# Kernel optimization log

Hardware: AMD Instinct MI355X
Metric: run time of the kernel (lower is better)

Reference implementation:

```python
import jax, jax.numpy as jnp
import numpy as np
from jax import lax

EPS = 1e-5  # BatchNorm2d default eps


def binarize(v):
    # Hubara sign binarization with straight-through estimator:
    # forward = sign(v) (sign(0)=+1), backward grad = 1_{|v|<=1}
    vc = jnp.clip(v, -1.0, 1.0)
    s = jnp.where(v >= 0, 1.0, -1.0).astype(v.dtype)
    return vc + lax.stop_gradient(s - vc)


def setup_inputs() -> dict:
    key = jax.random.key(0)
    k1, k2 = jax.random.split(key)
    x = jax.random.normal(k1, (32, 256, 56, 56), dtype=jnp.float32)
    W = jax.random.normal(k2, (256, 256, 3, 3), dtype=jnp.float32) * 0.05
    gamma = jnp.ones((256,), dtype=jnp.float32)
    beta = jnp.zeros((256,), dtype=jnp.float32)
    return {"x": x, "W": W, "gamma": gamma, "beta": beta}


def reference(x, W, gamma, beta):
    # BnnActivation: binarize input to {-1,+1}
    bx = binarize(x)
    # BnnConv2d: binarize weights, dilated conv (stride=1, padding=2, dilation=2)
    bw = binarize(W)
    y = lax.conv_general_dilated(
        bx, bw,
        window_strides=(1, 1),
        padding=((2, 2), (2, 2)),
        rhs_dilation=(2, 2),
        dimension_numbers=("NCHW", "OIHW", "NCHW"),
    )  # [N, C_out, H, W]
    # BatchNorm2d (training-mode batch statistics, affine)
    mean = jnp.mean(y, axis=(0, 2, 3))
    var = jnp.var(y, axis=(0, 2, 3))
    yn = (y - mean[None, :, None, None]) * lax.rsqrt(var + EPS)[None, :, None, None]
    yn = yn * gamma[None, :, None, None] + beta[None, :, None, None]
    return jnp.tanh(yn)
```

## Files before the change

### kernel.cpp

```cpp
#include <hip/hip_runtime.h>

typedef unsigned long long u64;
typedef unsigned int u32;
typedef unsigned short u16;
typedef int i32x4 __attribute__((ext_vector_type(4)));
typedef int i32x16 __attribute__((ext_vector_type(16)));

#define HW 3136
#define XPITCH 3600
#define NPPIX 115200
#define KTOT 2304
#define MT 128
#define NSTEP 36


__global__ __launch_bounds__(256) void pack_w_i8(const float* __restrict__ W,
                                                 char* __restrict__ wp,
                                                 u64* __restrict__ ssum) {
    int idx = blockIdx.x * 256 + threadIdx.x;
    if (blockIdx.x == 0) {
        ssum[threadIdx.x] = 0;
        ssum[threadIdx.x + 256] = 0;
    }
    int ci4 = idx & 63;
    int tapco = idx >> 6;
    int co = tapco / 9, tap = tapco % 9;
    u32 out = 0;
    #pragma unroll
    for (int k = 0; k < 4; ++k) {
        float v = W[((size_t)co * 256 + ci4 * 4 + k) * 9 + tap];
        out |= (v >= 0.f ? 0x01u : 0xFFu) << (8 * k);
    }
    int kc = tap * 16 + (ci4 >> 2);
    *(u32*)(wp + ((long)kc * 256 + co) * 16 + (ci4 & 3) * 4) = out;
}

__global__ __launch_bounds__(256) void pack_x_i8(const float* __restrict__ x,
                                                 char* __restrict__ xp) {
    int s = blockIdx.x * 256 + threadIdx.x;
    int word = blockIdx.y;
    int n = s / XPITCH, p = s % XPITCH;
    int h = p / 60, w = p % 60;
    bool inb = (h >= 2 && h < 58 && w >= 2 && w < 58);
    u64 b = 0;
    if (inb) {
        const float* px = x + ((size_t)(n * 256 + word * 64)) * HW + (h - 2) * 56 + (w - 2);
        #pragma unroll 8
        for (int ci = 0; ci < 64; ++ci) {
            float v = px[(size_t)ci * HW];
            if (v >= 0.f) b |= 1ull << ci;
        }
    }
    #pragma unroll
    for (int q = 0; q < 4; ++q) {
        u32 wds[4];
        #pragma unroll
        for (int j = 0; j < 4; ++j) {
            u32 bits = (u32)(b >> (q * 16 + j * 4)) & 15u;
            u32 t = (bits * 0x00204081u) & 0x01010101u;
            wds[j] = inb ? (~(t * 0xFEu)) : 0u;
        }
        *(uint4*)(xp + (((long)(word * 4 + q)) * NPPIX + s) * 16) =
            make_uint4(wds[0], wds[1], wds[2], wds[3]);
    }
}

__global__ __launch_bounds__(512) void conv_mfma(const char* __restrict__ xp,
                                                 const char* __restrict__ wp,
                                                 short* __restrict__ y) {
    __shared__ char lds[2][24576];
    int tid = threadIdx.x;
    int lane = tid & 63, wid = tid >> 6;
    int wm = wid & 1, wn = wid >> 1;
    long tile = blockIdx.x;

    int xrow = tid & 127, xlc = tid >> 7;
    long s0 = tile * MT + xrow;
    int xn = (int)(s0 / HW), xhw = (int)(s0 % HW);
    long xpix = (long)xn * XPITCH + (xhw / 56) * 60 + (xhw % 56);

    i32x16 acc00 = {}, acc01 = {}, acc10 = {}, acc11 = {};

#define STAGE(step, buf)                                                                  \
    {                                                                                     \
        int tap = (step) >> 2, q = (step) & 3;                                            \
        long shift = (long)((tap / 3) * 120 + (tap % 3) * 2);                             \
        long xaddr = (((long)(q * 4 + xlc)) * NPPIX + xpix + shift) * 16;                 \
        __builtin_amdgcn_global_load_lds(                                                 \
            (const __attribute__((address_space(1))) u32*)(xp + xaddr),                   \
            (__attribute__((address_space(3))) u32*)&lds[buf][wid * 1024], 16, 0, 0);     \
        _Pragma("unroll")                                                                 \
        for (int r = 0; r < 2; ++r) {                                                     \
            int L = r * 512 + tid;                                                        \
            long waddr = (((long)(tap * 16 + q * 4 + (L >> 8))) * 256 + (L & 255)) * 16;  \
            __builtin_amdgcn_global_load_lds(                                             \
                (const __attribute__((address_space(1))) u32*)(wp + waddr),               \
                (__attribute__((address_space(3))) u32*)&lds[buf][8192 + (r * 512 + wid * 64) * 16], \
                16, 0, 0);                                                                \
        }                                                                                 \
    }

#define COMPUTE(buf)                                                                      \
    {                                                                                     \
        _Pragma("unroll")                                                                 \
        for (int kc = 0; kc < 2; ++kc) {                                                  \
            int cx = kc * 2 + (lane >> 5);                                                \
            const char* xb = &lds[buf][cx * 2048 + (wm * 64 + (lane & 31)) * 16];         \
            const char* wb = &lds[buf][8192 + cx * 4096 + (wn * 64 + (lane & 31)) * 16];  \
            i32x4 xf0 = *(const i32x4*)xb;                                                \
            i32x4 xf1 = *(const i32x4*)(xb + 512);                                        \
            i32x4 wf0 = *(const i32x4*)wb;                                                \
            i32x4 wf1 = *(const i32x4*)(wb + 512);                                        \
            acc00 = __builtin_amdgcn_mfma_i32_32x32x32_i8(wf0, xf0, acc00, 0, 0, 0);      \
            acc01 = __builtin_amdgcn_mfma_i32_32x32x32_i8(wf0, xf1, acc01, 0, 0, 0);      \
            acc10 = __builtin_amdgcn_mfma_i32_32x32x32_i8(wf1, xf0, acc10, 0, 0, 0);      \
            acc11 = __builtin_amdgcn_mfma_i32_32x32x32_i8(wf1, xf1, acc11, 0, 0, 0);      \
        }                                                                                 \
    }

    STAGE(0, 0);
    __syncthreads();
    #pragma unroll 2
    for (int st = 0; st < NSTEP; ++st) {
        int cur = st & 1;
        if (st + 1 < NSTEP) STAGE(st + 1, cur ^ 1);
        COMPUTE(cur);
        __syncthreads();
    }
#undef STAGE
#undef COMPUTE

    #pragma unroll
    for (int jp = 0; jp < 2; ++jp) {
        long s = tile * MT + wm * 64 + jp * 32 + (lane & 31);
        int n = (int)(s / HW), hw = (int)(s % HW);
        short* yb = y + ((long)n * 256) * HW + hw;
        #pragma unroll
        for (int jc = 0; jc < 2; ++jc) {
            i32x16 A = jc ? (jp ? acc11 : acc10) : (jp ? acc01 : acc00);
            #pragma unroll
            for (int r = 0; r < 16; ++r) {
                int co = wn * 64 + jc * 32 + (r & 3) + 8 * (r >> 2) + 4 * (lane >> 5);
                yb[(long)co * HW] = (short)A[r];
            }
        }
    }
}


__global__ __launch_bounds__(256) void stats1_kernel(const short* __restrict__ y,
                                                     u64* __restrict__ ssum) {
    int pl = blockIdx.x;
    const short* p = y + (size_t)pl * HW;
    int tid = threadIdx.x;
    int a1 = 0; long long q1 = 0;
    for (int i = tid; i < 392; i += 256) {
        int4 v = *(const int4*)(p + i * 8);
        int vs[4] = {v.x, v.y, v.z, v.w};
        int a = 0, q = 0;
        #pragma unroll
        for (int j = 0; j < 4; ++j) {
            int lo = (short)(vs[j] & 0xffff);
            int hi = (short)(vs[j] >> 16);
            a += lo + hi;
            q += lo * lo + hi * hi;
        }
        a1 += a; q1 += q;
    }
    long long s1 = a1, s2 = q1;
    #pragma unroll
    for (int off = 32; off > 0; off >>= 1) {
        s1 += __shfl_down(s1, off);
        s2 += __shfl_down(s2, off);
    }
    __shared__ long long ls1[4], ls2[4];
    if ((tid & 63) == 0) { ls1[tid >> 6] = s1; ls2[tid >> 6] = s2; }
    __syncthreads();
    if (tid == 0) {
        long long S1 = ls1[0] + ls1[1] + ls1[2] + ls1[3];
        long long S2 = ls2[0] + ls2[1] + ls2[2] + ls2[3];
        int cch = pl & 255;
        atomicAdd(&ssum[cch],       (u64)S1);
        atomicAdd(&ssum[256 + cch], (u64)S2);
    }
}

__global__ __launch_bounds__(256) void norm_kernel(const short* __restrict__ y,
                                                   const u64* __restrict__ ssum,
                                                   const float* __restrict__ gamma,
                                                   const float* __restrict__ beta,
                                                   float* __restrict__ out) {
    size_t i = ((size_t)blockIdx.x * 256 + threadIdx.x) * 8;
    int cch = (int)((i / HW) & 255);
    double S1 = (double)(long long)ssum[cch];
    double S2 = (double)(long long)ssum[256 + cch];
    double mean = S1 / 100352.0;
    double var = S2 / 100352.0 - mean * mean;
    float a = gamma[cch] * rsqrtf((float)var + 1e-5f);
    float b = beta[cch] - (float)mean * a;

    int4 v = *(const int4*)(y + i);
    int vs[4] = {v.x, v.y, v.z, v.w};
    float r[8];
    #pragma unroll
    for (int j = 0; j < 4; ++j) {
        short lo = (short)(vs[j] & 0xffff);
        short hi = (short)(vs[j] >> 16);
        r[2 * j]     = tanhf(a * (float)lo + b);
        r[2 * j + 1] = tanhf(a * (float)hi + b);
    }
    *(float4*)(out + i)     = make_float4(r[0], r[1], r[2], r[3]);
    *(float4*)(out + i + 4) = make_float4(r[4], r[5], r[6], r[7]);
}


__global__ __launch_bounds__(256) void pack_w_kernel(const float* __restrict__ W,
                                                     u32* __restrict__ wp32,
                                                     u16* __restrict__ pw,
                                                     u64* __restrict__ ssum) {
    if (blockIdx.x == 0) {
        ssum[threadIdx.x] = 0;
        ssum[threadIdx.x + 256] = 0;
    }
    int t = blockIdx.x * 256 + threadIdx.x;
    int co = t / 9, tap = t % 9;
    u64 b[4] = {0, 0, 0, 0};
    for (int ci = 0; ci < 256; ++ci) {
        float v = W[(size_t)(co * 256 + ci) * 9 + tap];
        if (v >= 0.f) b[ci >> 6] |= 1ull << (ci & 63);
    }
    u32* dst = wp32 + ((size_t)tap * 256 + co) * 8;
    #pragma unroll
    for (int j = 0; j < 4; ++j) {
        dst[2 * j]     = (u32)b[j];
        dst[2 * j + 1] = (u32)(b[j] >> 32);
    }
    pw[co * 9 + tap] = (u16)(__popcll(b[0]) + __popcll(b[1]) + __popcll(b[2]) + __popcll(b[3]));
}

__global__ __launch_bounds__(256) void pack_x_kernel(const float* __restrict__ x,
                                                     u64* __restrict__ xpad,
                                                     const u16* __restrict__ pw,
                                                     u16* __restrict__ bias) {
    int s = blockIdx.x * 256 + threadIdx.x;
    int word = blockIdx.y;
    int n = s / XPITCH, p = s % XPITCH;
    int h = p / 60, w = p % 60;
    u64 b = 0;
    if (h >= 2 && h < 58 && w >= 2 && w < 58) {
        const float* px = x + ((size_t)(n * 256 + word * 64)) * HW + (h - 2) * 56 + (w - 2);
        #pragma unroll 8
        for (int ci = 0; ci < 64; ++ci) {
            float v = px[(size_t)ci * HW];
            if (v >= 0.f) b |= 1ull << ci;
        }
    }
    xpad[(size_t)s * 4 + word] = b;

    if (blockIdx.x == 0 && blockIdx.y == 0) {
        for (int i = threadIdx.x; i < 9 * 256; i += 256) {
            int mi = i >> 8, co = i & 255;
            int rm = mi / 3, cm = mi % 3;
            int vr = rm == 0 ? 6 : (rm == 2 ? 3 : 7);
            int vc = cm == 0 ? 6 : (cm == 2 ? 3 : 7);
            int corr = 0;
            for (int kh = 0; kh < 3; ++kh)
                for (int kw = 0; kw < 3; ++kw)
                    if (!(((vr >> kh) & 1) && ((vc >> kw) & 1)))
                        corr += pw[co * 9 + kh * 3 + kw];
            bias[mi * 256 + co] = (u16)(256 * __popc(vr) * __popc(vc) + 2 * corr);
        }
    }
}

#define CPT 8
__global__ __launch_bounds__(256) void conv_kernel(const u32* __restrict__ xpad,
                                                   const u32* __restrict__ wp32,
                                                   const u16* __restrict__ bias,
                                                   short* __restrict__ y) {
    int s = blockIdx.x * 256 + threadIdx.x;
    int n = s / HW, hw = s % HW;
    int h = hw / 56, w = hw % 56;
    int co0 = blockIdx.y * CPT;
    const u32* xb = xpad + ((size_t)n * XPITCH + h * 60 + w) * 8;
    uint4 xa[9], xc[9];
    #pragma unroll
    for (int kh = 0; kh < 3; ++kh)
        #pragma unroll
        for (int kw = 0; kw < 3; ++kw) {
            const u32* px = xb + (kh * 120 + kw * 2) * 8;
            xa[kh * 3 + kw] = *(const uint4*)(px);
            xc[kh * 3 + kw] = *(const uint4*)(px + 4);
        }
    int acc[CPT];
    #pragma unroll
    for (int cc = 0; cc < CPT; ++cc) acc[cc] = 0;
    #pragma unroll
    for (int t = 0; t < 9; ++t) {
        const u32* wt = wp32 + (((size_t)t * 256 + co0) * 8);
        uint4 a = xa[t], b = xc[t];
        #pragma unroll
        for (int cc = 0; cc < CPT; ++cc) {
            const u32* wc8 = wt + cc * 8;
            acc[cc] = __popc(a.x ^ wc8[0]) + acc[cc];
            acc[cc] = __popc(a.y ^ wc8[1]) + acc[cc];
            acc[cc] = __popc(a.z ^ wc8[2]) + acc[cc];
            acc[cc] = __popc(a.w ^ wc8[3]) + acc[cc];
            acc[cc] = __popc(b.x ^ wc8[4]) + acc[cc];
            acc[cc] = __popc(b.y ^ wc8[5]) + acc[cc];
            acc[cc] = __popc(b.z ^ wc8[6]) + acc[cc];
            acc[cc] = __popc(b.w ^ wc8[7]) + acc[cc];
        }
    }
    int rm = (h < 2) ? 0 : (h > 53 ? 2 : 1);
    int cm = (w < 2) ? 0 : (w > 53 ? 2 : 1);
    int mi = rm * 3 + cm;
    uint4 bv = *(const uint4*)(bias + (size_t)mi * 256 + co0);
    u32 bw[4] = {bv.x, bv.y, bv.z, bv.w};
    short* yo = y + ((size_t)n * 256 + co0) * HW + hw;
    #pragma unroll
    for (int cc = 0; cc < CPT; ++cc) {
        int bval = (int)((bw[cc >> 1] >> ((cc & 1) * 16)) & 0xffff);
        yo[(size_t)cc * HW] = (short)(bval - 2 * acc[cc]);
    }
}


extern "C" void kernel_launch(void* const* d_in, const int* in_sizes, int n_in,
                              void* d_out, int out_size, void* d_ws, size_t ws_size,
                              hipStream_t stream) {
    const float* x     = (const float*)d_in[0];
    const float* W     = (const float*)d_in[1];
    const float* gamma = (const float*)d_in[2];
    const float* beta  = (const float*)d_in[3];
    float* out = (float*)d_out;
    char* ws = (char*)d_ws;

    short* y = (short*)ws;

    if (ws_size >= 81465344) {
        char* xi8 = ws + 51380224;
        char* wi8 = ws + 80871424;
        u64* ssum = (u64*)(ws + 81461248);
        pack_w_i8<<<576, 256, 0, stream>>>(W, wi8, ssum);
        pack_x_i8<<<dim3(450, 4), 256, 0, stream>>>(x, xi8);
        conv_mfma<<<784, 512, 0, stream>>>(xi8, wi8, y);
        stats1_kernel<<<8192, 256, 0, stream>>>(y, ssum);
        norm_kernel<<<12544, 256, 0, stream>>>(y, ssum, gamma, beta, out);
    } else {
        u64* xpad = (u64*)(ws + 51380224);
        u32* wp32 = (u32*)(ws + 55066624);
        u16* pw   = (u16*)(ws + 55140352);
        u16* bias = (u16*)(ws + 55144960);
        u64* ssum = (u64*)(ws + 55149568);
        pack_w_kernel<<<9, 256, 0, stream>>>(W, wp32, pw, ssum);
        pack_x_kernel<<<dim3(450, 4), 256, 0, stream>>>(x, xpad, pw, bias);
        conv_kernel<<<dim3(392, 32), 256, 0, stream>>>((const u32*)xpad, wp32, bias, y);
        stats1_kernel<<<8192, 256, 0, stream>>>(y, ssum);
        norm_kernel<<<12544, 256, 0, stream>>>(y, ssum, gamma, beta, out);
    }
}
```

Measured before the change: 140.8 us.

## Fuse BN statistics into conv epilogue and deepen load pipeline with manual waitcnt

The conv kernel now computes per-channel sum and sum-of-squares from its int accumulators with lane shuffles and atomics, so the separate stats kernel no longer re-reads y. The main loop is also restructured to keep two stages in flight, using explicit vmcnt/lgkmcnt waits and raw s_barrier in place of __syncthreads. The pipelining relies on the STAGE macro issuing exactly the load count that vmcnt(3) assumes, which is fragile, and the epilogue adds many global atomics.

Result: slower. 283.7 us (+101.5%).

```diff
diff --git a/kernel.cpp b/kernel.cpp
--- a/kernel.cpp
+++ b/kernel.cpp
@@ -67,7 +67,8 @@
 
 __global__ __launch_bounds__(512) void conv_mfma(const char* __restrict__ xp,
                                                  const char* __restrict__ wp,
-                                                 short* __restrict__ y) {
+                                                 short* __restrict__ y,
+                                                 u64* __restrict__ ssum) {
     __shared__ char lds[2][24576];
     int tid = threadIdx.x;
     int lane = tid & 63, wid = tid >> 6;
@@ -119,16 +120,23 @@
     }
 
     STAGE(0, 0);
-    __syncthreads();
+    STAGE(1, 1);
     #pragma unroll 2
-    for (int st = 0; st < NSTEP; ++st) {
+    for (int st = 0; st < NSTEP - 1; ++st) {
         int cur = st & 1;
-        if (st + 1 < NSTEP) STAGE(st + 1, cur ^ 1);
+        asm volatile("s_waitcnt vmcnt(3)" ::: "memory");
+        __builtin_amdgcn_s_barrier();
+        __builtin_amdgcn_sched_barrier(0);
         COMPUTE(cur);
-        __syncthreads();
-    }
-#undef STAGE
-#undef COMPUTE
+        __builtin_amdgcn_sched_barrier(0);
+        asm volatile("s_waitcnt lgkmcnt(0)" ::: "memory");
+        __builtin_amdgcn_s_barrier();
+        if (st + 2 < NSTEP) STAGE(st + 2, cur);
+    }
+    asm volatile("s_waitcnt vmcnt(0)" ::: "memory");
+    __builtin_amdgcn_s_barrier();
+    __builtin_amdgcn_sched_barrier(0);
+    COMPUTE((NSTEP - 1) & 1);
 
     #pragma unroll
     for (int jp = 0; jp < 2; ++jp) {
@@ -145,45 +153,29 @@
             }
         }
     }
-}
-
-
-__global__ __launch_bounds__(256) void stats1_kernel(const short* __restrict__ y,
-                                                     u64* __restrict__ ssum) {
-    int pl = blockIdx.x;
-    const short* p = y + (size_t)pl * HW;
-    int tid = threadIdx.x;
-    int a1 = 0; long long q1 = 0;
-    for (int i = tid; i < 392; i += 256) {
-        int4 v = *(const int4*)(p + i * 8);
-        int vs[4] = {v.x, v.y, v.z, v.w};
-        int a = 0, q = 0;
-        #pragma unroll
-        for (int j = 0; j < 4; ++j) {
-            int lo = (short)(vs[j] & 0xffff);
-            int hi = (short)(vs[j] >> 16);
-            a += lo + hi;
-            q += lo * lo + hi * hi;
-        }
-        a1 += a; q1 += q;
-    }
-    long long s1 = a1, s2 = q1;
-    #pragma unroll
-    for (int off = 32; off > 0; off >>= 1) {
-        s1 += __shfl_down(s1, off);
-        s2 += __shfl_down(s2, off);
-    }
-    __shared__ long long ls1[4], ls2[4];
-    if ((tid & 63) == 0) { ls1[tid >> 6] = s1; ls2[tid >> 6] = s2; }
-    __syncthreads();
-    if (tid == 0) {
-        long long S1 = ls1[0] + ls1[1] + ls1[2] + ls1[3];
-        long long S2 = ls2[0] + ls2[1] + ls2[2] + ls2[3];
-        int cch = pl & 255;
-        atomicAdd(&ssum[cch],       (u64)S1);
-        atomicAdd(&ssum[256 + cch], (u64)S2);
-    }
-}
+
+    #pragma unroll
+    for (int jc = 0; jc < 2; ++jc) {
+        i32x16 A0 = jc ? acc10 : acc00;
+        i32x16 A1 = jc ? acc11 : acc01;
+        #pragma unroll
+        for (int r = 0; r < 16; ++r) {
+            int v = A0[r] + A1[r];
+            int q = A0[r] * A0[r] + A1[r] * A1[r];
+            #pragma unroll
+            for (int off = 16; off > 0; off >>= 1) {
+                v += __shfl_xor(v, off);
+                q += __shfl_xor(q, off);
+            }
+            if ((lane & 31) == 0) {
+                int co = wn * 64 + jc * 32 + (r & 3) + 8 * (r >> 2) + 4 * (lane >> 5);
+                atomicAdd(&ssum[co],       (u64)(long long)v);
+                atomicAdd(&ssum[256 + co], (u64)(long long)q);
+            }
+        }
+    }
+}
+
 
 __global__ __launch_bounds__(256) void norm_kernel(const short* __restrict__ y,
                                                    const u64* __restrict__ ssum,
@@ -211,6 +203,43 @@
     }
     *(float4*)(out + i)     = make_float4(r[0], r[1], r[2], r[3]);
     *(float4*)(out + i + 4) = make_float4(r[4], r[5], r[6], r[7]);
+}
+
+__global__ __launch_bounds__(256) void stats1_kernel(const short* __restrict__ y,
+                                                     u64* __restrict__ ssum) {
+    int pl = blockIdx.x;
+    const short* p = y + (size_t)pl * HW;
+    int tid = threadIdx.x;
+    int a1 = 0; long long q1 = 0;
+    for (int i = tid; i < 392; i += 256) {
+        int4 v = *(const int4*)(p + i * 8);
+        int vs[4] = {v.x, v.y, v.z, v.w};
+        int a = 0, q = 0;
+        #pragma unroll
+        for (int j = 0; j < 4; ++j) {
+            int lo = (short)(vs[j] & 0xffff);
+            int hi = (short)(vs[j] >> 16);
+            a += lo + hi;
+            q += lo * lo + hi * hi;
+        }
+        a1 += a; q1 += q;
+    }
+    long long s1 = a1, s2 = q1;
+    #pragma unroll
+    for (int off = 32; off > 0; off >>= 1) {
+        s1 += __shfl_down(s1, off);
+        s2 += __shfl_down(s2, off);
+    }
+    __shared__ long long ls1[4], ls2[4];
+    if ((tid & 63) == 0) { ls1[tid >> 6] = s1; ls2[tid >> 6] = s2; }
+    __syncthreads();
+    if (tid == 0) {
+        long long S1 = ls1[0] + ls1[1] + ls1[2] + ls1[3];
+        long long S2 = ls2[0] + ls2[1] + ls2[2] + ls2[3];
+        int cch = pl & 255;
+        atomicAdd(&ssum[cch],       (u64)S1);
+        atomicAdd(&ssum[256 + cch], (u64)S2);
+    }
 }
 
 
@@ -344,8 +373,7 @@
         u64* ssum = (u64*)(ws + 81461248);
         pack_w_i8<<<576, 256, 0, stream>>>(W, wi8, ssum);
         pack_x_i8<<<dim3(450, 4), 256, 0, stream>>>(x, xi8);
-        conv_mfma<<<784, 512, 0, stream>>>(xi8, wi8, y);
-        stats1_kernel<<<8192, 256, 0, stream>>>(y, ssum);
+        conv_mfma<<<784, 512, 0, stream>>>(xi8, wi8, y, ssum);
         norm_kernel<<<12544, 256, 0, stream>>>(y, ssum, gamma, beta, out);
     } else {
         u64* xpad = (u64*)(ws + 51380224);
```

## Merge pack kernels and read conv weights directly from global memory

Applied to the files above, without the earlier changes.

The two packing kernels are combined into a single launch, with the block index selecting x-packing or weight-packing work, which saves one kernel launch. The conv kernel no longer stages weight tiles into LDS; each lane loads its weight fragments straight from global memory, relying on L2/L1 caching because all 784 blocks share the same weights. This shrinks LDS use from 48KB to 16KB per block, which may raise occupancy, but puts global load latency on the MFMA critical path without prefetching.

Result: slower. 147.0 us (+4.4%).

```diff
diff --git a/kernel.cpp b/kernel.cpp
--- a/kernel.cpp
+++ b/kernel.cpp
@@ -14,61 +14,64 @@
 #define NSTEP 36
 
 
-__global__ __launch_bounds__(256) void pack_w_i8(const float* __restrict__ W,
-                                                 char* __restrict__ wp,
-                                                 u64* __restrict__ ssum) {
-    int idx = blockIdx.x * 256 + threadIdx.x;
-    if (blockIdx.x == 0) {
-        ssum[threadIdx.x] = 0;
-        ssum[threadIdx.x + 256] = 0;
-    }
-    int ci4 = idx & 63;
-    int tapco = idx >> 6;
-    int co = tapco / 9, tap = tapco % 9;
-    u32 out = 0;
-    #pragma unroll
-    for (int k = 0; k < 4; ++k) {
-        float v = W[((size_t)co * 256 + ci4 * 4 + k) * 9 + tap];
-        out |= (v >= 0.f ? 0x01u : 0xFFu) << (8 * k);
-    }
-    int kc = tap * 16 + (ci4 >> 2);
-    *(u32*)(wp + ((long)kc * 256 + co) * 16 + (ci4 & 3) * 4) = out;
-}
-
-__global__ __launch_bounds__(256) void pack_x_i8(const float* __restrict__ x,
-                                                 char* __restrict__ xp) {
-    int s = blockIdx.x * 256 + threadIdx.x;
-    int word = blockIdx.y;
-    int n = s / XPITCH, p = s % XPITCH;
-    int h = p / 60, w = p % 60;
-    bool inb = (h >= 2 && h < 58 && w >= 2 && w < 58);
-    u64 b = 0;
-    if (inb) {
-        const float* px = x + ((size_t)(n * 256 + word * 64)) * HW + (h - 2) * 56 + (w - 2);
-        #pragma unroll 8
-        for (int ci = 0; ci < 64; ++ci) {
-            float v = px[(size_t)ci * HW];
-            if (v >= 0.f) b |= 1ull << ci;
-        }
-    }
-    #pragma unroll
-    for (int q = 0; q < 4; ++q) {
-        u32 wds[4];
-        #pragma unroll
-        for (int j = 0; j < 4; ++j) {
-            u32 bits = (u32)(b >> (q * 16 + j * 4)) & 15u;
-            u32 t = (bits * 0x00204081u) & 0x01010101u;
-            wds[j] = inb ? (~(t * 0xFEu)) : 0u;
-        }
-        *(uint4*)(xp + (((long)(word * 4 + q)) * NPPIX + s) * 16) =
-            make_uint4(wds[0], wds[1], wds[2], wds[3]);
+__global__ __launch_bounds__(256) void pack_all(const float* __restrict__ x,
+                                                const float* __restrict__ W,
+                                                char* __restrict__ xp,
+                                                char* __restrict__ wp,
+                                                u64* __restrict__ ssum) {
+    int bx = blockIdx.x;
+    if (bx < 1800) {
+        int word = bx / 450;
+        int s = (bx % 450) * 256 + threadIdx.x;
+        int n = s / XPITCH, p = s % XPITCH;
+        int h = p / 60, w = p % 60;
+        bool inb = (h >= 2 && h < 58 && w >= 2 && w < 58);
+        u64 b = 0;
+        if (inb) {
+            const float* px = x + ((size_t)(n * 256 + word * 64)) * HW + (h - 2) * 56 + (w - 2);
+            #pragma unroll 8
+            for (int ci = 0; ci < 64; ++ci) {
+                float v = px[(size_t)ci * HW];
+                if (v >= 0.f) b |= 1ull << ci;
+            }
+        }
+        #pragma unroll
+        for (int q = 0; q < 4; ++q) {
+            u32 wds[4];
+            #pragma unroll
+            for (int j = 0; j < 4; ++j) {
+                u32 bits = (u32)(b >> (q * 16 + j * 4)) & 15u;
+                u32 t = (bits * 0x00204081u) & 0x01010101u;
+                wds[j] = inb ? (~(t * 0xFEu)) : 0u;
+            }
+            *(uint4*)(xp + (((long)(word * 4 + q)) * NPPIX + s) * 16) =
+                make_uint4(wds[0], wds[1], wds[2], wds[3]);
+        }
+    } else {
+        int bi = bx - 1800;
+        if (bi == 0) {
+            ssum[threadIdx.x] = 0;
+            ssum[threadIdx.x + 256] = 0;
+        }
+        int idx = bi * 256 + threadIdx.x;
+        int ci4 = idx & 63;
+        int tapco = idx >> 6;
+        int co = tapco / 9, tap = tapco % 9;
+        u32 out = 0;
+        #pragma unroll
+        for (int k = 0; k < 4; ++k) {
+            float v = W[((size_t)co * 256 + ci4 * 4 + k) * 9 + tap];
+            out |= (v >= 0.f ? 0x01u : 0xFFu) << (8 * k);
+        }
+        int kc = tap * 16 + (ci4 >> 2);
+        *(u32*)(wp + ((long)kc * 256 + co) * 16 + (ci4 & 3) * 4) = out;
     }
 }
 
 __global__ __launch_bounds__(512) void conv_mfma(const char* __restrict__ xp,
                                                  const char* __restrict__ wp,
                                                  short* __restrict__ y) {
-    __shared__ char lds[2][24576];
+    __shared__ char lds[2][8192];
     int tid = threadIdx.x;
     int lane = tid & 63, wid = tid >> 6;
     int wm = wid & 1, wn = wid >> 1;
@@ -89,24 +92,17 @@
         __builtin_amdgcn_global_load_lds(                                                 \
             (const __attribute__((address_space(1))) u32*)(xp + xaddr),                   \
             (__attribute__((address_space(3))) u32*)&lds[buf][wid * 1024], 16, 0, 0);     \
-        _Pragma("unroll")                                                                 \
-        for (int r = 0; r < 2; ++r) {                                                     \
-            int L = r * 512 + tid;                                                        \
-            long waddr = (((long)(tap * 16 + q * 4 + (L >> 8))) * 256 + (L & 255)) * 16;  \
-            __builtin_amdgcn_global_load_lds(                                             \
-                (const __attribute__((address_space(1))) u32*)(wp + waddr),               \
-                (__attribute__((address_space(3))) u32*)&lds[buf][8192 + (r * 512 + wid * 64) * 16], \
-                16, 0, 0);                                                                \
-        }                                                                                 \
-    }
-
-#define COMPUTE(buf)                                                                      \
+    }
+
+#define COMPUTE(step, buf)                                                                \
     {                                                                                     \
+        int tap = (step) >> 2, q = (step) & 3;                                            \
         _Pragma("unroll")                                                                 \
         for (int kc = 0; kc < 2; ++kc) {                                                  \
             int cx = kc * 2 + (lane >> 5);                                                \
             const char* xb = &lds[buf][cx * 2048 + (wm * 64 + (lane & 31)) * 16];         \
-            const char* wb = &lds[buf][8192 + cx * 4096 + (wn * 64 + (lane & 31)) * 16];  \
+            const char* wb = wp + ((long)(tap * 16 + q * 4 + cx) * 256                    \
+                                   + wn * 64 + (lane & 31)) * 16;                         \
             i32x4 xf0 = *(const i32x4*)xb;                                                \
             i32x4 xf1 = *(const i32x4*)(xb + 512);                                        \
             i32x4 wf0 = *(const i32x4*)wb;                                                \
@@ -124,7 +120,7 @@
     for (int st = 0; st < NSTEP; ++st) {
         int cur = st & 1;
         if (st + 1 < NSTEP) STAGE(st + 1, cur ^ 1);
-        COMPUTE(cur);
+        COMPUTE(st, cur);
         __syncthreads();
     }
 #undef STAGE
@@ -342,8 +338,7 @@
         char* xi8 = ws + 51380224;
         char* wi8 = ws + 80871424;
         u64* ssum = (u64*)(ws + 81461248);
-        pack_w_i8<<<576, 256, 0, stream>>>(W, wi8, ssum);
-        pack_x_i8<<<dim3(450, 4), 256, 0, stream>>>(x, xi8);
+        pack_all<<<2376, 256, 0, stream>>>(x, W, xi8, wi8, ssum);
         conv_mfma<<<784, 512, 0, stream>>>(xi8, wi8, y);
         stats1_kernel<<<8192, 256, 0, stream>>>(y, ssum);
         norm_kernel<<<12544, 256, 0, stream>>>(y, ssum, gamma, beta, out);
```
